# Performance work log

Hardware: AMD Instinct MI355X
Metric: run time of the kernel (lower is better)

Reference implementation:

```python
import jax, jax.numpy as jnp
import numpy as np

N_NODES = 10000
HEADS = 4
HID = 64
EPS_BN = 1e-5
NEG_SLOPE = 0.2


def gat_conv(x, W, att_src, att_dst, bias, src, dst, heads, out_c, concat):
    """PyG-style GATConv (eval mode, self-loops already appended).
    x: [N, F_in], W: [F_in, heads*out_c], att_*: [heads, out_c], bias: [heads*out_c] or [out_c].
    """
    N = x.shape[0]
    h = (x @ W).reshape(N, heads, out_c)                      # [N,H,C]
    a_s = jnp.sum(h * att_src, axis=-1)                       # [N,H]
    a_d = jnp.sum(h * att_dst, axis=-1)                       # [N,H]
    logits = jax.nn.leaky_relu(a_s[src] + a_d[dst], NEG_SLOPE)  # [E,H]
    # segment softmax over incoming edges of each dst node
    m = jax.ops.segment_max(logits, dst, num_segments=N)
    m = jnp.where(jnp.isfinite(m), m, 0.0)
    e = jnp.exp(logits - m[dst])
    s = jax.ops.segment_sum(e, dst, num_segments=N)
    alpha = e / (s[dst] + 1e-16)                              # [E,H]
    out = jax.ops.segment_sum(h[src] * alpha[..., None], dst, num_segments=N)  # [N,H,C]
    if concat:
        out = out.reshape(N, heads * out_c)
    else:
        out = out.mean(axis=1)
    return out + bias


def batch_norm_eval(x, gamma, beta, mean, var):
    return gamma * (x - mean) * jax.lax.rsqrt(var + EPS_BN) + beta


def setup_inputs() -> dict:
    key = jax.random.key(0)
    ks = jax.random.split(key, 16)
    N, E = N_NODES, 320000
    in_c, hid, H, out_c = 128, HID, HEADS, 64
    x = jax.random.normal(ks[0], (N, in_c), dtype=jnp.float32)
    edge_index = jax.random.randint(ks[1], (2, E), 0, N, dtype=jnp.int32)

    def glorot(k, shape):
        fan = shape[0] + shape[-1]
        return jax.random.normal(k, shape, dtype=jnp.float32) * jnp.sqrt(2.0 / fan)

    return {
        "x": x, "edge_index": edge_index,
        "W0": glorot(ks[2], (in_c, H * hid)),
        "att_src0": glorot(ks[3], (H, hid)), "att_dst0": glorot(ks[4], (H, hid)),
        "b0": jnp.zeros((H * hid,), jnp.float32),
        "g0": jax.random.uniform(ks[5], (H * hid,), jnp.float32, 0.5, 1.5),
        "be0": jax.random.normal(ks[6], (H * hid,), jnp.float32) * 0.1,
        "m0": jnp.zeros((H * hid,), jnp.float32), "v0": jnp.ones((H * hid,), jnp.float32),
        "W1": glorot(ks[7], (H * hid, H * hid)),
        "att_src1": glorot(ks[8], (H, hid)), "att_dst1": glorot(ks[9], (H, hid)),
        "b1": jnp.zeros((H * hid,), jnp.float32),
        "g1": jax.random.uniform(ks[10], (H * hid,), jnp.float32, 0.5, 1.5),
        "be1": jax.random.normal(ks[11], (H * hid,), jnp.float32) * 0.1,
        "m1": jnp.zeros((H * hid,), jnp.float32), "v1": jnp.ones((H * hid,), jnp.float32),
        # layer 2: 256 -> 64, heads=1, concat=False
        "W2": glorot(ks[12], (H * hid, out_c)),
        "att_src2": glorot(ks[13], (1, out_c)), "att_dst2": glorot(ks[14], (1, out_c)),
        "b2": jnp.zeros((out_c,), jnp.float32),
    }


def reference(x, edge_index, W0, att_src0, att_dst0, b0, g0, be0, m0, v0,
              W1, att_src1, att_dst1, b1, g1, be1, m1, v1,
              W2, att_src2, att_dst2, b2):
    N = x.shape[0]
    loops = jnp.arange(N, dtype=edge_index.dtype)
    src = jnp.concatenate([edge_index[0], loops])  # PyG add_self_loops
    dst = jnp.concatenate([edge_index[1], loops])

    h = gat_conv(x, W0, att_src0, att_dst0, b0, src, dst, HEADS, HID, True)
    h = jax.nn.elu(h)
    h = batch_norm_eval(h, g0, be0, m0, v0)

    h = gat_conv(h, W1, att_src1, att_dst1, b1, src, dst, HEADS, HID, True)
    h = jax.nn.elu(h)
    h = batch_norm_eval(h, g1, be1, m1, v1)

    h = gat_conv(h, W2, att_src2, att_dst2, b2, src, dst, 1, 64, False)
    return jax.nn.log_softmax(h, axis=1)
```

## Files before the change

kernel.cpp:

```cpp
#include <hip/hip_runtime.h>
#include <cstdint>
#include <cstddef>

#define NNODES 10000
#define NEDGES 320000
#define NPAD   10048
#define NBLK   157
#define CAP    128

#define BW0  128
#define BW1  256
#define BW2  64
#define BSC  1250

typedef unsigned short ushort_t;
typedef short bf16x8 __attribute__((ext_vector_type(8)));
typedef float f32x4 __attribute__((ext_vector_type(4)));

__device__ __forceinline__ float lrelu(float x) { return x > 0.f ? x : 0.2f * x; }
__device__ __forceinline__ ushort_t f2b(float v) {
  unsigned b = __float_as_uint(v);
  b += 0x7fffu + ((b >> 16) & 1u);
  return (ushort_t)(b >> 16);
}
__device__ __forceinline__ float blo(unsigned u) { return __uint_as_float(u << 16); }
__device__ __forceinline__ float bhi(unsigned u) { return __uint_as_float(u & 0xffff0000u); }
__device__ __forceinline__ bf16x8 cvt8(const float* p) {
  bf16x8 r;
#pragma unroll
  for (int i = 0; i < 8; ++i) r[i] = (short)f2b(p[i]);
  return r;
}

__global__ __launch_bounds__(256) void prep_kernel(
    const float* __restrict__ W0, const float* __restrict__ W1, const float* __restrict__ W2,
    const int* __restrict__ ei,
    ushort_t* __restrict__ WT0, ushort_t* __restrict__ WT1, ushort_t* __restrict__ WT2,
    int* __restrict__ cursor, int* __restrict__ srcsPad) {
  int b = blockIdx.x;
  int tid = threadIdx.x;
  if (b < BW0) { int i = b * 256 + tid; int k = i >> 8, m = i & 255; WT0[m * 128 + k] = f2b(W0[i]); return; }
  b -= BW0;
  if (b < BW1) { int i = b * 256 + tid; int k = i >> 8, m = i & 255; WT1[m * 256 + k] = f2b(W1[i]); return; }
  b -= BW1;
  if (b < BW2) { int i = b * 256 + tid; int k = i >> 6, m = i & 63; WT2[m * 256 + k] = f2b(W2[i]); return; }
  b -= BW2;
  {
    int e = b * 256 + tid;
    int s = ei[e], d = ei[NEDGES + e];
    int slot = atomicAdd(&cursor[d], 1);
    srcsPad[d * CAP + slot] = s;
  }
}

__global__ __launch_bounds__(256) void gemm0_kernel(
    const float* __restrict__ x,
    const ushort_t* __restrict__ WT,
    const float* __restrict__ atts, const float* __restrict__ attd,
    ushort_t* __restrict__ hb,
    float* __restrict__ a_s, float* __restrict__ a_d) {
  const int K = 128, M = 256;
  int tid = threadIdx.x, wave = tid >> 6, lane = tid & 63;
  int quad = lane >> 4, l16 = lane & 15;
  int n0 = blockIdx.x * 64, head = blockIdx.y, m0 = head * 64;
  int row = n0 + wave * 16 + l16;
  int rowc = row < NNODES ? row : NNODES - 1;
  f32x4 acc[4];
#pragma unroll
  for (int t = 0; t < 4; ++t) acc[t] = (f32x4){0.f, 0.f, 0.f, 0.f};
  const float* Ap = x + (size_t)rowc * K + quad * 8;
  const ushort_t* Wp = WT + (size_t)(m0 + l16) * K + quad * 8;
  for (int k0 = 0; k0 < K; k0 += 32) {
    bf16x8 af = cvt8(Ap + k0);
#pragma unroll
    for (int t = 0; t < 4; ++t) {
      bf16x8 bf = *(const bf16x8*)(Wp + (size_t)t * 16 * K + k0);
      acc[t] = __builtin_amdgcn_mfma_f32_16x16x32_bf16(af, bf, acc[t], 0, 0, 0);
    }
  }
#pragma unroll
  for (int reg = 0; reg < 4; ++reg) {
    int r = n0 + wave * 16 + quad * 4 + reg;
    float ps = 0.f, pd = 0.f;
#pragma unroll
    for (int t = 0; t < 4; ++t) {
      float v = acc[t][reg];
      int col = m0 + t * 16 + l16;
      ps = fmaf(v, atts[col], ps);
      pd = fmaf(v, attd[col], pd);
      if (r < NNODES) hb[(size_t)r * M + col] = f2b(v);
    }
#pragma unroll
    for (int off = 8; off; off >>= 1) {
      ps += __shfl_xor(ps, off);
      pd += __shfl_xor(pd, off);
    }
    if (l16 == 0 && r < NNODES) {
      a_s[r * 4 + head] = ps;
      a_d[r * 4 + head] = pd;
    }
  }
}

template <int H>
__global__ __launch_bounds__(256) void gemm_att_kernel(
    const ushort_t* __restrict__ Ab,
    const ushort_t* __restrict__ WT,
    const float* __restrict__ atts, const float* __restrict__ attd,
    ushort_t* __restrict__ hb, float* __restrict__ a_s, float* __restrict__ a_d) {
  const int K = 256, M = H * 64;
  int tid = threadIdx.x, wave = tid >> 6, lane = tid & 63;
  int quad = lane >> 4, l16 = lane & 15;
  int n0 = blockIdx.x * 64, head = blockIdx.y, m0 = head * 64;
  int row = n0 + wave * 16 + l16;
  int rowc = row < NNODES ? row : NNODES - 1;
  f32x4 acc[4];
#pragma unroll
  for (int t = 0; t < 4; ++t) acc[t] = (f32x4){0.f, 0.f, 0.f, 0.f};
  const ushort_t* Ap = Ab + (size_t)rowc * K + quad * 8;
  const ushort_t* Wp = WT + (size_t)(m0 + l16) * K + quad * 8;
  for (int k0 = 0; k0 < K; k0 += 32) {
    bf16x8 af = *(const bf16x8*)(Ap + k0);
#pragma unroll
    for (int t = 0; t < 4; ++t) {
      bf16x8 bf = *(const bf16x8*)(Wp + (size_t)t * 16 * K + k0);
      acc[t] = __builtin_amdgcn_mfma_f32_16x16x32_bf16(af, bf, acc[t], 0, 0, 0);
    }
  }
#pragma unroll
  for (int reg = 0; reg < 4; ++reg) {
    int r = n0 + wave * 16 + quad * 4 + reg;
    float ps = 0.f, pd = 0.f;
#pragma unroll
    for (int t = 0; t < 4; ++t) {
      float v = acc[t][reg];
      int col = m0 + t * 16 + l16;
      ps = fmaf(v, atts[col], ps);
      pd = fmaf(v, attd[col], pd);
      if (r < NNODES) hb[(size_t)r * M + col] = f2b(v);
    }
#pragma unroll
    for (int off = 8; off; off >>= 1) {
      ps += __shfl_xor(ps, off);
      pd += __shfl_xor(pd, off);
    }
    if (l16 == 0 && r < NNODES) {
      a_s[r * H + head] = ps;
      a_d[r * H + head] = pd;
    }
  }
}

__device__ __forceinline__ void gather8_full(const char* base, const float* alds,
                                             const int* olds, int esub, float acc[8]) {
#pragma unroll
  for (int it = 0; it < 8; ++it) {
    int e = it * 8 + esub;
    float a = alds[e];
    int o = olds[e];
    uint4 q = *(const uint4*)(base + o);
    acc[0] = fmaf(a, blo(q.x), acc[0]); acc[1] = fmaf(a, bhi(q.x), acc[1]);
    acc[2] = fmaf(a, blo(q.y), acc[2]); acc[3] = fmaf(a, bhi(q.y), acc[3]);
    acc[4] = fmaf(a, blo(q.z), acc[4]); acc[5] = fmaf(a, bhi(q.z), acc[5]);
    acc[6] = fmaf(a, blo(q.w), acc[6]); acc[7] = fmaf(a, bhi(q.w), acc[7]);
  }
}

__device__ __forceinline__ void gather8(const char* base, const float* alds, const int* olds,
                                        int cnt, int esub, float acc[8]) {
  int iters = (cnt + 7) >> 3;
  for (int it = 0; it < iters; ++it) {
    int e = it * 8 + esub;
    float a = alds[e];
    int o = olds[e];
    uint4 q = *(const uint4*)(base + o);
    acc[0] = fmaf(a, blo(q.x), acc[0]); acc[1] = fmaf(a, bhi(q.x), acc[1]);
    acc[2] = fmaf(a, blo(q.y), acc[2]); acc[3] = fmaf(a, bhi(q.y), acc[3]);
    acc[4] = fmaf(a, blo(q.z), acc[4]); acc[5] = fmaf(a, bhi(q.z), acc[5]);
    acc[6] = fmaf(a, blo(q.w), acc[6]); acc[7] = fmaf(a, bhi(q.w), acc[7]);
  }
}

__global__ __launch_bounds__(256) void aggregate_kernel(
    const ushort_t* __restrict__ hb16, const float* __restrict__ a_s,
    const float* __restrict__ a_d,
    const int* __restrict__ cursor, const int* __restrict__ srcsPad,
    const float* __restrict__ bias, const float* __restrict__ gam, const float* __restrict__ bet,
    const float* __restrict__ rmean, const float* __restrict__ rvar,
    ushort_t* __restrict__ xb16) {
  __shared__ float s_alpha[4][64];
  __shared__ int s_off[4][64];
  int n = blockIdx.x;
  int hh = threadIdx.x >> 6;
  int lane = threadIdx.x & 63;
  int esub = lane >> 3, csub = lane & 7;
  float* alds = s_alpha[hh];
  int* olds = s_off[hh];
  int degi = cursor[n];
  int dtot = degi + 1;
  float adn = a_d[n * 4 + hh];
  const char* base = (const char*)hb16 + hh * 128 + csub * 16;
  float acc[8];
#pragma unroll
  for (int i = 0; i < 8; ++i) acc[i] = 0.f;

  if (dtot <= 64) {
    int s = (lane < degi) ? srcsPad[n * CAP + lane] : n;
    float l = (lane < dtot) ? lrelu(a_s[s * 4 + hh] + adn) : -1e30f;
    float mx = l;
#pragma unroll
    for (int off = 32; off; off >>= 1) mx = fmaxf(mx, __shfl_xor(mx, off));
    float e = (lane < dtot) ? __expf(l - mx) : 0.f;
    float sum = e;
#pragma unroll
    for (int off = 32; off; off >>= 1) sum += __shfl_xor(sum, off);
    alds[lane] = e / (sum + 1e-16f);
    olds[lane] = s * 512;
    gather8_full(base, alds, olds, esub, acc);
  } else {
    float mx = -1e30f;
    for (int j = lane; j < dtot; j += 64) {
      int s = (j < degi) ? srcsPad[n * CAP + j] : n;
      mx = fmaxf(mx, lrelu(a_s[s * 4 + hh] + adn));
    }
#pragma unroll
    for (int off = 32; off; off >>= 1) mx = fmaxf(mx, __shfl_xor(mx, off));
    float sum = 0.f;
    for (int j = lane; j < dtot; j += 64) {
      int s = (j < degi) ? srcsPad[n * CAP + j] : n;
      sum += __expf(lrelu(a_s[s * 4 + hh] + adn) - mx);
    }
#pragma unroll
    for (int off = 32; off; off >>= 1) sum += __shfl_xor(sum, off);
    float inv = 1.0f / (sum + 1e-16f);
    for (int j0 = 0; j0 < dtot; j0 += 64) {
      int cnt = min(64, dtot - j0);
      int j = j0 + lane;
      int s = (j < degi) ? srcsPad[n * CAP + j] : n;
      alds[lane] = (lane < cnt) ? __expf(lrelu(a_s[s * 4 + hh] + adn) - mx) * inv : 0.f;
      olds[lane] = s * 512;
      gather8(base, alds, olds, cnt, esub, acc);
    }
  }

#pragma unroll
  for (int i = 0; i < 8; ++i) {
    acc[i] += __shfl_xor(acc[i], 8);
    acc[i] += __shfl_xor(acc[i], 16);
    acc[i] += __shfl_xor(acc[i], 32);
  }
  if (esub == 0) {
    int col0 = hh * 64 + csub * 8;
    float4 bi0 = *(const float4*)&bias[col0],  bi1 = *(const float4*)&bias[col0 + 4];
    float4 gm0 = *(const float4*)&gam[col0],   gm1 = *(const float4*)&gam[col0 + 4];
    float4 bt0 = *(const float4*)&bet[col0],   bt1 = *(const float4*)&bet[col0 + 4];
    float4 rm0 = *(const float4*)&rmean[col0], rm1 = *(const float4*)&rmean[col0 + 4];
    float4 rv0 = *(const float4*)&rvar[col0],  rv1 = *(const float4*)&rvar[col0 + 4];
    float bi[8] = {bi0.x, bi0.y, bi0.z, bi0.w, bi1.x, bi1.y, bi1.z, bi1.w};
    float gm[8] = {gm0.x, gm0.y, gm0.z, gm0.w, gm1.x, gm1.y, gm1.z, gm1.w};
    float bt[8] = {bt0.x, bt0.y, bt0.z, bt0.w, bt1.x, bt1.y, bt1.z, bt1.w};
    float rm[8] = {rm0.x, rm0.y, rm0.z, rm0.w, rm1.x, rm1.y, rm1.z, rm1.w};
    float rv[8] = {rv0.x, rv0.y, rv0.z, rv0.w, rv1.x, rv1.y, rv1.z, rv1.w};
    unsigned pk[4];
#pragma unroll
    for (int i = 0; i < 4; ++i) {
      float v0 = acc[2 * i] + bi[2 * i], v1 = acc[2 * i + 1] + bi[2 * i + 1];
      v0 = v0 > 0.f ? v0 : (__expf(v0) - 1.f);
      v1 = v1 > 0.f ? v1 : (__expf(v1) - 1.f);
      v0 = fmaf(gm[2 * i] * (v0 - rm[2 * i]), rsqrtf(rv[2 * i] + 1e-5f), bt[2 * i]);
      v1 = fmaf(gm[2 * i + 1] * (v1 - rm[2 * i + 1]), rsqrtf(rv[2 * i + 1] + 1e-5f), bt[2 * i + 1]);
      pk[i] = (unsigned)f2b(v0) | ((unsigned)f2b(v1) << 16);
    }
    *(uint4*)((char*)xb16 + (size_t)n * 512 + col0 * 2) = make_uint4(pk[0], pk[1], pk[2], pk[3]);
  }
}

__global__ __launch_bounds__(256) void aggregate2_kernel(
    const ushort_t* __restrict__ hb16, const float* __restrict__ a_s,
    const float* __restrict__ a_d,
    const int* __restrict__ cursor, const int* __restrict__ srcsPad,
    const float* __restrict__ bias, float* __restrict__ out) {
  __shared__ float s_alpha[4][64];
  __shared__ int s_off[4][64];
  int wave = threadIdx.x >> 6;
  int n = blockIdx.x * 4 + wave;
  int lane = threadIdx.x & 63;
  int esub = lane >> 3, csub = lane & 7;
  if (n >= NNODES) return;
  float* alds = s_alpha[wave];
  int* olds = s_off[wave];
  int degi = cursor[n];
  int dtot = degi + 1;
  float adn = a_d[n];
  const char* base = (const char*)hb16 + csub * 16;
  float acc[8];
#pragma unroll
  for (int i = 0; i < 8; ++i) acc[i] = 0.f;

  if (dtot <= 64) {
    int s = (lane < degi) ? srcsPad[n * CAP + lane] : n;
    float l = (lane < dtot) ? lrelu(a_s[s] + adn) : -1e30f;
    float mx = l;
#pragma unroll
    for (int off = 32; off; off >>= 1) mx = fmaxf(mx, __shfl_xor(mx, off));
    float e = (lane < dtot) ? __expf(l - mx) : 0.f;
    float sum = e;
#pragma unroll
    for (int off = 32; off; off >>= 1) sum += __shfl_xor(sum, off);
    alds[lane] = e / (sum + 1e-16f);
    olds[lane] = s * 128;
    gather8_full(base, alds, olds, esub, acc);
  } else {
    float mx = -1e30f;
    for (int j = lane; j < dtot; j += 64) {
      int s = (j < degi) ? srcsPad[n * CAP + j] : n;
      mx = fmaxf(mx, lrelu(a_s[s] + adn));
    }
#pragma unroll
    for (int off = 32; off; off >>= 1) mx = fmaxf(mx, __shfl_xor(mx, off));
    float sum = 0.f;
    for (int j = lane; j < dtot; j += 64) {
      int s = (j < degi) ? srcsPad[n * CAP + j] : n;
      sum += __expf(lrelu(a_s[s] + adn) - mx);
    }
#pragma unroll
    for (int off = 32; off; off >>= 1) sum += __shfl_xor(sum, off);
    float inv = 1.0f / (sum + 1e-16f);
    for (int j0 = 0; j0 < dtot; j0 += 64) {
      int cnt = min(64, dtot - j0);
      int j = j0 + lane;
      int s = (j < degi) ? srcsPad[n * CAP + j] : n;
      alds[lane] = (lane < cnt) ? __expf(lrelu(a_s[s] + adn) - mx) * inv : 0.f;
      olds[lane] = s * 128;
      gather8(base, alds, olds, cnt, esub, acc);
    }
  }

#pragma unroll
  for (int i = 0; i < 8; ++i) {
    acc[i] += __shfl_xor(acc[i], 8);
    acc[i] += __shfl_xor(acc[i], 16);
    acc[i] += __shfl_xor(acc[i], 32);
  }
  int col0 = csub * 8;
  float4 bi0 = *(const float4*)&bias[col0], bi1 = *(const float4*)&bias[col0 + 4];
  float v[8] = {acc[0] + bi0.x, acc[1] + bi0.y, acc[2] + bi0.z, acc[3] + bi0.w,
                acc[4] + bi1.x, acc[5] + bi1.y, acc[6] + bi1.z, acc[7] + bi1.w};
  float mx = v[0];
#pragma unroll
  for (int i = 1; i < 8; ++i) mx = fmaxf(mx, v[i]);
#pragma unroll
  for (int off = 4; off; off >>= 1) mx = fmaxf(mx, __shfl_xor(mx, off));
  float ex = 0.f;
#pragma unroll
  for (int i = 0; i < 8; ++i) ex += __expf(v[i] - mx);
#pragma unroll
  for (int off = 4; off; off >>= 1) ex += __shfl_xor(ex, off);
  float lse = mx + logf(ex);
  if (esub == 0) {
    float4 o0 = make_float4(v[0] - lse, v[1] - lse, v[2] - lse, v[3] - lse);
    float4 o1 = make_float4(v[4] - lse, v[5] - lse, v[6] - lse, v[7] - lse);
    *(float4*)&out[(size_t)n * 64 + col0] = o0;
    *(float4*)&out[(size_t)n * 64 + col0 + 4] = o1;
  }
}

extern "C" void kernel_launch(void* const* d_in, const int* in_sizes, int n_in,
                              void* d_out, int out_size, void* d_ws, size_t ws_size,
                              hipStream_t stream) {
  const float* x = (const float*)d_in[0];
  const int* ei = (const int*)d_in[1];
  const float* W0 = (const float*)d_in[2];
  const float* as0 = (const float*)d_in[3];
  const float* ad0 = (const float*)d_in[4];
  const float* b0 = (const float*)d_in[5];
  const float* g0p = (const float*)d_in[6];
  const float* be0 = (const float*)d_in[7];
  const float* m0p = (const float*)d_in[8];
  const float* v0p = (const float*)d_in[9];
  const float* W1 = (const float*)d_in[10];
  const float* as1 = (const float*)d_in[11];
  const float* ad1 = (const float*)d_in[12];
  const float* b1 = (const float*)d_in[13];
  const float* g1p = (const float*)d_in[14];
  const float* be1 = (const float*)d_in[15];
  const float* m1p = (const float*)d_in[16];
  const float* v1p = (const float*)d_in[17];
  const float* W2 = (const float*)d_in[18];
  const float* as2 = (const float*)d_in[19];
  const float* ad2 = (const float*)d_in[20];
  const float* b2 = (const float*)d_in[21];
  float* out = (float*)d_out;

  char* w = (char*)d_ws;
  auto alloc = [&](size_t bytes) {
    void* r = (void*)w;
    w += (bytes + 255) & ~(size_t)255;
    return r;
  };
  ushort_t* hb = (ushort_t*)alloc((size_t)NNODES * 256 * 2);
  ushort_t* xb = (ushort_t*)alloc((size_t)NNODES * 256 * 2);
  ushort_t* WT0 = (ushort_t*)alloc((size_t)256 * 128 * 2);
  ushort_t* WT1 = (ushort_t*)alloc((size_t)256 * 256 * 2);
  ushort_t* WT2 = (ushort_t*)alloc((size_t)64 * 256 * 2);
  float* a_s = (float*)alloc((size_t)NNODES * 4 * 4);
  float* a_d = (float*)alloc((size_t)NNODES * 4 * 4);
  int* cursor = (int*)alloc((size_t)NNODES * 4);
  int* srcsPad = (int*)alloc((size_t)NNODES * CAP * 4);

  hipMemsetAsync(cursor, 0, (size_t)NNODES * 4, stream);
  prep_kernel<<<BW0 + BW1 + BW2 + BSC, 256, 0, stream>>>(
      W0, W1, W2, ei, WT0, WT1, WT2, cursor, srcsPad);
  gemm0_kernel<<<dim3(NBLK, 4), 256, 0, stream>>>(x, WT0, as0, ad0, hb, a_s, a_d);
  aggregate_kernel<<<NNODES, 256, 0, stream>>>(hb, a_s, a_d, cursor, srcsPad,
                                               b0, g0p, be0, m0p, v0p, xb);
  gemm_att_kernel<4><<<dim3(NBLK, 4), 256, 0, stream>>>(xb, WT1, as1, ad1, hb, a_s, a_d);
  aggregate_kernel<<<NNODES, 256, 0, stream>>>(hb, a_s, a_d, cursor, srcsPad,
                                               b1, g1p, be1, m1p, v1p, xb);
  gemm_att_kernel<1><<<dim3(NBLK, 1), 256, 0, stream>>>(xb, WT2, as2, ad2, hb, a_s, a_d);
  aggregate2_kernel<<<(NNODES + 3) / 4, 256, 0, stream>>>(hb, a_s, a_d, cursor, srcsPad,
                                                          b2, out);
}
```

Before: 234.7 us.

## Store per-head feature planes and remap aggregate blocks to head-major groups

The GEMM kernels now write the projected features in a head-major layout ([head][node][64]) instead of node-major rows of 256. The aggregation kernel is remapped so each block handles one head for four nodes, with the block index interleaved so that a block group covers two node quads across all four heads. The intent is that each gather touches a 10000x128-byte head plane, which fits better in cache and improves locality for the random source rows. It costs a more complex block-to-node mapping, and the host launch (not shown) must match the new grid.

```diff
diff --git a/kernel.cpp b/kernel.cpp
--- a/kernel.cpp
+++ b/kernel.cpp
@@ -57,9 +57,9 @@
     const float* __restrict__ x,
     const ushort_t* __restrict__ WT,
     const float* __restrict__ atts, const float* __restrict__ attd,
-    ushort_t* __restrict__ hb,
+    ushort_t* __restrict__ hbH,
     float* __restrict__ a_s, float* __restrict__ a_d) {
-  const int K = 128, M = 256;
+  const int K = 128;
   int tid = threadIdx.x, wave = tid >> 6, lane = tid & 63;
   int quad = lane >> 4, l16 = lane & 15;
   int n0 = blockIdx.x * 64, head = blockIdx.y, m0 = head * 64;
@@ -88,7 +88,7 @@
       int col = m0 + t * 16 + l16;
       ps = fmaf(v, atts[col], ps);
       pd = fmaf(v, attd[col], pd);
-      if (r < NNODES) hb[(size_t)r * M + col] = f2b(v);
+      if (r < NNODES) hbH[(size_t)(head * NNODES + r) * 64 + t * 16 + l16] = f2b(v);
     }
 #pragma unroll
     for (int off = 8; off; off >>= 1) {
@@ -107,8 +107,8 @@
     const ushort_t* __restrict__ Ab,
     const ushort_t* __restrict__ WT,
     const float* __restrict__ atts, const float* __restrict__ attd,
-    ushort_t* __restrict__ hb, float* __restrict__ a_s, float* __restrict__ a_d) {
-  const int K = 256, M = H * 64;
+    ushort_t* __restrict__ hbH, float* __restrict__ a_s, float* __restrict__ a_d) {
+  const int K = 256;
   int tid = threadIdx.x, wave = tid >> 6, lane = tid & 63;
   int quad = lane >> 4, l16 = lane & 15;
   int n0 = blockIdx.x * 64, head = blockIdx.y, m0 = head * 64;
@@ -137,7 +137,7 @@
       int col = m0 + t * 16 + l16;
       ps = fmaf(v, atts[col], ps);
       pd = fmaf(v, attd[col], pd);
-      if (r < NNODES) hb[(size_t)r * M + col] = f2b(v);
+      if (r < NNODES) hbH[(size_t)(head * NNODES + r) * 64 + t * 16 + l16] = f2b(v);
     }
 #pragma unroll
     for (int off = 8; off; off >>= 1) {
@@ -182,7 +182,7 @@
 }
 
 __global__ __launch_bounds__(256) void aggregate_kernel(
-    const ushort_t* __restrict__ hb16, const float* __restrict__ a_s,
+    const ushort_t* __restrict__ hbH, const float* __restrict__ a_s,
     const float* __restrict__ a_d,
     const int* __restrict__ cursor, const int* __restrict__ srcsPad,
     const float* __restrict__ bias, const float* __restrict__ gam, const float* __restrict__ bet,
@@ -190,23 +190,27 @@
     ushort_t* __restrict__ xb16) {
   __shared__ float s_alpha[4][64];
   __shared__ int s_off[4][64];
-  int n = blockIdx.x;
-  int hh = threadIdx.x >> 6;
+  int g = blockIdx.x;
+  int xx = g & 7;
+  int head = xx & 3;
+  int group = (g >> 3) * 2 + (xx >> 2);
+  int wave = threadIdx.x >> 6;
+  int n = group * 4 + wave;
   int lane = threadIdx.x & 63;
   int esub = lane >> 3, csub = lane & 7;
-  float* alds = s_alpha[hh];
-  int* olds = s_off[hh];
+  float* alds = s_alpha[wave];
+  int* olds = s_off[wave];
   int degi = cursor[n];
   int dtot = degi + 1;
-  float adn = a_d[n * 4 + hh];
-  const char* base = (const char*)hb16 + hh * 128 + csub * 16;
+  float adn = a_d[n * 4 + head];
+  const char* base = (const char*)hbH + (size_t)head * NNODES * 128 + csub * 16;
   float acc[8];
 #pragma unroll
   for (int i = 0; i < 8; ++i) acc[i] = 0.f;
 
   if (dtot <= 64) {
     int s = (lane < degi) ? srcsPad[n * CAP + lane] : n;
-    float l = (lane < dtot) ? lrelu(a_s[s * 4 + hh] + adn) : -1e30f;
+    float l = (lane < dtot) ? lrelu(a_s[s * 4 + head] + adn) : -1e30f;
     float mx = l;
 #pragma unroll
     for (int off = 32; off; off >>= 1) mx = fmaxf(mx, __shfl_xor(mx, off));
@@ -215,20 +219,20 @@
 #pragma unroll
     for (int off = 32; off; off >>= 1) sum += __shfl_xor(sum, off);
     alds[lane] = e / (sum + 1e-16f);
-    olds[lane] = s * 512;
+    olds[lane] = s * 128;
     gather8_full(base, alds, olds, esub, acc);
   } else {
     float mx = -1e30f;
     for (int j = lane; j < dtot; j += 64) {
       int s = (j < degi) ? srcsPad[n * CAP + j] : n;
-      mx = fmaxf(mx, lrelu(a_s[s * 4 + hh] + adn));
+      mx = fmaxf(mx, lrelu(a_s[s * 4 + head] + adn));
     }
 #pragma unroll
     for (int off = 32; off; off >>= 1) mx = fmaxf(mx, __shfl_xor(mx, off));
     float sum = 0.f;
     for (int j = lane; j < dtot; j += 64) {
       int s = (j < degi) ? srcsPad[n * CAP + j] : n;
-      sum += __expf(lrelu(a_s[s * 4 + hh] + adn) - mx);
+      sum += __expf(lrelu(a_s[s * 4 + head] + adn) - mx);
     }
 #pragma unroll
     for (int off = 32; off; off >>= 1) sum += __shfl_xor(sum, off);
@@ -237,8 +241,8 @@
       int cnt = min(64, dtot - j0);
       int j = j0 + lane;
       int s = (j < degi) ? srcsPad[n * CAP + j] : n;
-      alds[lane] = (lane < cnt) ? __expf(lrelu(a_s[s * 4 + hh] + adn) - mx) * inv : 0.f;
-      olds[lane] = s * 512;
+      alds[lane] = (lane < cnt) ? __expf(lrelu(a_s[s * 4 + head] + adn) - mx) * inv : 0.f;
+      olds[lane] = s * 128;
       gather8(base, alds, olds, cnt, esub, acc);
     }
   }
@@ -250,7 +254,7 @@
     acc[i] += __shfl_xor(acc[i], 32);
   }
   if (esub == 0) {
-    int col0 = hh * 64 + csub * 8;
+    int col0 = head * 64 + csub * 8;
     float4 bi0 = *(const float4*)&bias[col0],  bi1 = *(const float4*)&bias[col0 + 4];
     float4 gm0 = *(const float4*)&gam[col0],   gm1 = *(const float4*)&gam[col0 + 4];
     float4 bt0 = *(const float4*)&bet[col0],   bt1 = *(const float4*)&bet[col0 + 4];
@@ -276,8 +280,8 @@
 }
 
 __global__ __launch_bounds__(256) void aggregate2_kernel(
-    const ushort_t* __restrict__ hb16, const float* __restrict__ a_s,
-    const float* __restrict__ a_d,
+    const ushort_t* __restrict__ hb16,
+    const float* __restrict__ a_s, const float* __restrict__ a_d,
     const int* __restrict__ cursor, const int* __restrict__ srcsPad,
     const float* __restrict__ bias, float* __restrict__ out) {
   __shared__ float s_alpha[4][64];
```

Result: slower. 240.2 us (+2.4%).
